# Optimization experiments

Hardware: AMD Instinct MI355X
Metric: run time of the kernel (lower is better)

## Reference

```python
import jax, jax.numpy as jnp
import numpy as np

N, E, C = 50000, 10000, 500
NNZ = 400000
IN_DIM, EDGE_DIM, NODE_DIM, COMP_DIM = 128, 128, 128, 128


def _glorot(key, shape):
    fan = shape[0] + shape[1]
    return jax.random.normal(key, shape, jnp.float32) * (2.0 / fan) ** 0.5


def _seg_mean(vals, idx, num):
    # mean aggregation over segments (scatter-add + count normalize)
    s = jax.ops.segment_sum(vals, idx, num_segments=num)
    cnt = jax.ops.segment_sum(jnp.ones((idx.shape[0], 1), vals.dtype), idx, num_segments=num)
    return s / jnp.maximum(cnt, 1.0)


def _prelu(v, a):
    return jnp.where(v >= 0, v, a * v)


def _conv(x, ni, ei, ec_e, ec_c, nc_n, nc_c, n_nodes, n_edges, n_comps,
          Wne, Wen, Wec, Wnc, a):
    # node -> hyperedge message passing
    e = _seg_mean((x @ Wne)[ni], ei, n_edges)            # [E, edge_dim]
    e_act = _prelu(e, a)
    # hyperedge -> node
    n = _seg_mean((e_act @ Wen)[ei], ni, n_nodes)        # [N, node_dim]
    # edge -> component and node -> component
    c = _seg_mean((e_act @ Wec)[ec_e], ec_c, n_comps) + \
        _seg_mean((x @ Wnc)[nc_n], nc_c, n_comps)        # [C, comp_dim]
    return n, e, c


def setup_inputs() -> dict:
    key = jax.random.key(0)
    ks = jax.random.split(key, 16)
    x = jax.random.normal(ks[0], (N, IN_DIM), jnp.float32)
    hyperedge_index = jnp.stack([
        jax.random.randint(ks[1], (NNZ,), 0, N),
        jax.random.randint(ks[2], (NNZ,), 0, E),
    ])
    hyperedge_component_index = jnp.stack([
        jnp.arange(E), jax.random.randint(ks[3], (E,), 0, C)])
    node_component_index = jnp.stack([
        jnp.arange(N), jax.random.randint(ks[4], (N,), 0, C)])
    return dict(
        x=x,
        hyperedge_index=hyperedge_index,
        hyperedge_component_index=hyperedge_component_index,
        node_component_index=node_component_index,
        num_nodes=N, num_edges=E, num_components=C,
        W_ne0=_glorot(ks[5], (IN_DIM, EDGE_DIM)),
        W_en0=_glorot(ks[6], (EDGE_DIM, NODE_DIM)),
        W_ec0=_glorot(ks[7], (EDGE_DIM, COMP_DIM)),
        W_nc0=_glorot(ks[8], (IN_DIM, COMP_DIM)),
        W_ne1=_glorot(ks[9], (NODE_DIM, EDGE_DIM)),
        W_en1=_glorot(ks[10], (EDGE_DIM, NODE_DIM)),
        W_ec1=_glorot(ks[11], (EDGE_DIM, COMP_DIM)),
        W_nc1=_glorot(ks[12], (NODE_DIM, COMP_DIM)),
        prelu_a=jnp.array(0.25, jnp.float32),
    )


def reference(x, hyperedge_index, hyperedge_component_index, node_component_index,
              num_nodes, num_edges, num_components,
              W_ne0, W_en0, W_ec0, W_nc0, W_ne1, W_en1, W_ec1, W_nc1, prelu_a):
    ni, ei = hyperedge_index[0], hyperedge_index[1]
    ec_e, ec_c = hyperedge_component_index[0], hyperedge_component_index[1]
    nc_n, nc_c = node_component_index[0], node_component_index[1]
    layers = [(W_ne0, W_en0, W_ec0, W_nc0), (W_ne1, W_en1, W_ec1, W_nc1)]
    e_out = c_out = None
    for Wne, Wen, Wec, Wnc in layers:
        n_out, e_out, c_out = _conv(x, ni, ei, ec_e, ec_c, nc_n, nc_c,
                                    num_nodes, num_edges, num_components,
                                    Wne, Wen, Wec, Wnc, prelu_a)
        x = _prelu(n_out, prelu_a)  # HyperEncoder applies act between/after layers
    return (x, e_out, c_out)
```

## Files before the change

### kernel.cpp

```cpp
#include <hip/hip_runtime.h>
#include <stdint.h>

typedef unsigned int u32;
typedef _Float16 f16;
typedef f16 half8 __attribute__((ext_vector_type(8)));
typedef float f32x4 __attribute__((ext_vector_type(4)));
#define TS 4096
#define KB2 256
#define CH 2048

__device__ __forceinline__ float bflo(u32 u) { return __uint_as_float(u << 16); }
__device__ __forceinline__ float bfhi(u32 u) { return __uint_as_float(u & 0xffff0000u); }
__device__ __forceinline__ u32 f2bf(float x) {
    u32 u = __float_as_uint(x);
    return (u + 0x7fffu + ((u >> 16) & 1u)) >> 16;
}
__device__ __forceinline__ u32 pack2(float a, float b) { return f2bf(a) | (f2bf(b) << 16); }

__device__ __forceinline__ int bstart2(int b, int total) {
    return (int)(((unsigned long long)b * (u32)total + KB2 - 1) / KB2);
}

__device__ __forceinline__ int blk_exscan(int v, int& total) {
    __shared__ int ws[5];
    int t = threadIdx.x, lane = t & 63, w = t >> 6;
    int inc = v;
    for (int d = 1; d < 64; d <<= 1) { int u = __shfl_up(inc, d, 64); if (lane >= d) inc += u; }
    __syncthreads();
    if (lane == 63) ws[w] = inc;
    __syncthreads();
    if (t == 0) { int acc = 0; for (int i = 0; i < 4; ++i) { int x = ws[i]; ws[i] = acc; acc += x; } ws[4] = acc; }
    __syncthreads();
    total = ws[4];
    return ws[w] + (inc - v);
}

#define ACC8(v) do { \
    a[0] += bflo((v).x); a[1] += bfhi((v).x); a[2] += bflo((v).y); a[3] += bfhi((v).y); \
    a[4] += bflo((v).z); a[5] += bfhi((v).z); a[6] += bflo((v).w); a[7] += bfhi((v).w); } while (0)

__device__ __forceinline__ void seg_mean8(const u32* __restrict__ in,
                                          const int* __restrict__ items,
                                          const int* __restrict__ off,
                                          int nseg, int nrows, int seg, float a[8]) {
    int lane = threadIdx.x & 63;
    int rs = lane >> 4;
    int cc = lane & 15;
#pragma unroll
    for (int i = 0; i < 8; ++i) a[i] = 0.f;
    int s0 = 0, s1 = 0;
    if (seg < nseg) { s0 = off[seg]; s1 = off[seg + 1]; }
    const uint4* rows = (const uint4*)in;
    int base = s0;
    for (; base + 16 <= s1; base += 16) {
        u32 r0 = (u32)items[base + rs];
        u32 r1 = (u32)items[base + 4 + rs];
        u32 r2 = (u32)items[base + 8 + rs];
        u32 r3 = (u32)items[base + 12 + rs];
        r0 = (r0 < (u32)nrows) ? r0 : 0u;
        r1 = (r1 < (u32)nrows) ? r1 : 0u;
        r2 = (r2 < (u32)nrows) ? r2 : 0u;
        r3 = (r3 < (u32)nrows) ? r3 : 0u;
        uint4 v0 = rows[(size_t)r0 * 16 + cc];
        uint4 v1 = rows[(size_t)r1 * 16 + cc];
        uint4 v2 = rows[(size_t)r2 * 16 + cc];
        uint4 v3 = rows[(size_t)r3 * 16 + cc];
        ACC8(v0); ACC8(v1); ACC8(v2); ACC8(v3);
    }
    for (; base + 8 <= s1; base += 8) {
        u32 r0 = (u32)items[base + rs];
        u32 r1 = (u32)items[base + 4 + rs];
        r0 = (r0 < (u32)nrows) ? r0 : 0u;
        r1 = (r1 < (u32)nrows) ? r1 : 0u;
        uint4 v0 = rows[(size_t)r0 * 16 + cc];
        uint4 v1 = rows[(size_t)r1 * 16 + cc];
        ACC8(v0); ACC8(v1);
    }
    int idx = base + rs;
    if (idx < s1) {
        u32 r = (u32)items[idx]; r = (r < (u32)nrows) ? r : 0u;
        uint4 v = rows[(size_t)r * 16 + cc];
        ACC8(v);
    }
    idx += 4;
    if (idx < s1) {
        u32 r = (u32)items[idx]; r = (r < (u32)nrows) ? r : 0u;
        uint4 v = rows[(size_t)r * 16 + cc];
        ACC8(v);
    }
#pragma unroll
    for (int i = 0; i < 8; ++i) {
        a[i] += __shfl_xor(a[i], 16, 64);
        a[i] += __shfl_xor(a[i], 32, 64);
    }
    float inv = 1.f / fmaxf((float)(s1 - s0), 1.f);
#pragma unroll
    for (int i = 0; i < 8; ++i) a[i] *= inv;
}

__device__ __forceinline__ void agg4_body(const u32* __restrict__ in,
                                          const int* __restrict__ items,
                                          const int* __restrict__ off,
                                          float* __restrict__ out_f32,
                                          u32* __restrict__ out_bf,
                                          int nseg, int nrows, int do_prelu,
                                          const float* __restrict__ alpha_p, int seg) {
    if (seg >= nseg) return;
    int lane = threadIdx.x & 63;
    int rs = lane >> 4;
    int cc = lane & 15;
    float a[8];
    seg_mean8(in, items, off, nseg, nrows, seg, a);
    if (do_prelu) {
        float al = *alpha_p;
#pragma unroll
        for (int i = 0; i < 8; ++i) a[i] = (a[i] >= 0.f) ? a[i] : al * a[i];
    }
    if (rs == 0) {
        if (out_f32) {
            float* o = out_f32 + ((size_t)seg << 7) + cc * 8;
            *(float4*)o       = make_float4(a[0], a[1], a[2], a[3]);
            *(float4*)(o + 4) = make_float4(a[4], a[5], a[6], a[7]);
        }
        if (out_bf) {
            uint4 pk;
            pk.x = pack2(a[0], a[1]); pk.y = pack2(a[2], a[3]);
            pk.z = pack2(a[4], a[5]); pk.w = pack2(a[6], a[7]);
            *(uint4*)(out_bf + ((size_t)seg << 6) + cc * 4) = pk;
        }
    }
}

__global__ __launch_bounds__(256) void k_front(
        const float2* __restrict__ xin, u32* __restrict__ xout, int npairs,
        const int* __restrict__ ni, const int* __restrict__ ei,
        const int* __restrict__ nc_c, const int* __restrict__ ec_c,
        int* __restrict__ bcntE, int* __restrict__ bcntN,
        int* __restrict__ cnt_cn, int* __restrict__ cnt_ce,
        int nnz, int n, int e, int nbh, int nkc,
        int* __restrict__ ticket,
        int* __restrict__ basesE, int* __restrict__ basesN,
        int* __restrict__ bcur_e, int* __restrict__ bcur_n,
        int* __restrict__ off_cn, int* __restrict__ off_ce,
        int* __restrict__ cur_cn, int* __restrict__ cur_ce, int c,
        const float* __restrict__ W0, const float* __restrict__ W1,
        const float* __restrict__ W2, const float* __restrict__ W3,
        const float* __restrict__ W4, const float* __restrict__ W5,
        f16* __restrict__ wt6) {
    int t = threadIdx.x;
    int b = blockIdx.x;
    if (b >= nbh + nkc) {
        int gid = (b - nbh - nkc) * 256 + t;
        if (gid >= 6 * 2048) return;
        int m = gid >> 11;
        int rem = gid & 2047;
        int cq = rem >> 4;
        int s = rem & 15;
        const float* W = (m == 0) ? W0 : (m == 1) ? W1 : (m == 2) ? W2 :
                         (m == 3) ? W3 : (m == 4) ? W4 : W5;
        int khi = ((s & 7) ^ (cq & 7)) | (s & 8);
        int k0 = khi << 3;
        union { f16 h[8]; uint4 v; } u;
#pragma unroll
        for (int j = 0; j < 8; ++j) u.h[j] = (f16)W[((k0 + j) << 7) + cq];
        *(uint4*)(wt6 + ((size_t)m << 14) + (cq << 7) + (s << 3)) = u.v;
        return;
    }
    if (b >= nbh) {
        int j = (b - nbh) * 256 + t;
        if (j < npairs) { float2 v = xin[j]; xout[j] = pack2(v.x, v.y); }
        return;
    }
    __shared__ int hE[KB2], hN[KB2];
    __shared__ int lastflag;
    hE[t] = 0; hN[t] = 0;
    __syncthreads();
    int base = b * CH;
    int lim = base + CH; if (lim > nnz) lim = nnz;
    for (int i = base + t; i < lim; i += 256) {
        u32 v = (u32)ni[i], eg = (u32)ei[i];
        if (v >= (u32)n) v = 0;
        if (eg >= (u32)e) eg = 0;
        atomicAdd(&hE[(int)(((unsigned long long)eg * KB2) / (u32)e)], 1);
        atomicAdd(&hN[(int)(((unsigned long long)v  * KB2) / (u32)n)], 1);
    }
    __syncthreads();
    if (hE[t]) atomicAdd(&bcntE[t], hE[t]);
    if (hN[t]) atomicAdd(&bcntN[t], hN[t]);
    int gid = b * 256 + t, stride = nbh * 256;
    for (int j = gid; j < n + e; j += stride) {
        if (j < n) atomicAdd(&cnt_cn[nc_c[j]], 1);
        else       atomicAdd(&cnt_ce[ec_c[j - n]], 1);
    }
    __syncthreads();
    if (t == 0) {
        __threadfence();
        lastflag = (atomicAdd(ticket, 1) == nbh - 1);
    }
    __syncthreads();
    if (!lastflag) return;
    __threadfence();
    int tot;
    int v = bcntE[t];
    int ex = blk_exscan(v, tot);
    basesE[t] = ex; bcur_e[t] = ex;
    if (t == 0) basesE[KB2] = tot;
    v = bcntN[t];
    ex = blk_exscan(v, tot);
    basesN[t] = ex; bcur_n[t] = ex;
    if (t == 0) basesN[KB2] = tot;
    int i0 = 2 * t, i1 = 2 * t + 1;
    int v0 = (i0 < c) ? cnt_cn[i0] : 0;
    int v1 = (i1 < c) ? cnt_cn[i1] : 0;
    ex = blk_exscan(v0 + v1, tot);
    if (i0 < c) { off_cn[i0] = ex;      cur_cn[i0] = ex; }
    if (i1 < c) { off_cn[i1] = ex + v0; cur_cn[i1] = ex + v0; }
    if (t == 0) off_cn[c] = tot;
    v0 = (i0 < c) ? cnt_ce[i0] : 0;
    v1 = (i1 < c) ? cnt_ce[i1] : 0;
    ex = blk_exscan(v0 + v1, tot);
    if (i0 < c) { off_ce[i0] = ex;      cur_ce[i0] = ex; }
    if (i1 < c) { off_ce[i1] = ex + v0; cur_ce[i1] = ex + v0; }
    if (t == 0) off_ce[c] = tot;
}

__global__ __launch_bounds__(256) void k_part_a(
        const int* __restrict__ ni, const int* __restrict__ ei,
        int* __restrict__ bcur_e, int* __restrict__ bcur_n,
        u32* __restrict__ stg_e, u32* __restrict__ stg_n,
        const int* __restrict__ nc_n, const int* __restrict__ nc_c,
        const int* __restrict__ ec_e, const int* __restrict__ ec_c,
        int* __restrict__ cur_cn, int* __restrict__ cur_ce,
        int* __restrict__ csr_cn, int* __restrict__ csr_ce,
        int nnz, int n, int e) {
    __shared__ u32 pk[CH];
    __shared__ unsigned short bb[CH];
    __shared__ int hist[KB2];
    __shared__ int gb[KB2];
    int side = blockIdx.y;
    int base = blockIdx.x * CH;
    int cnt  = nnz - base; if (cnt > CH) cnt = CH;
    int t = threadIdx.x;
    for (int i = t; i < KB2; i += 256) hist[i] = 0;
    __syncthreads();
    u32 total = side ? (u32)n : (u32)e;
    for (int i = t; i < cnt; i += 256) {
        int v = ni[base + i], eg = ei[base + i];
        u32 key = side ? (u32)v : (u32)eg;
        u32 pay = side ? (u32)eg : (u32)v;
        if (key >= total) key = 0;
        u32 b = (u32)(((unsigned long long)key * KB2) / total);
        pk[i] = side ? (pay | (key << 14)) : (pay | (key << 16));
        bb[i] = (unsigned short)b;
        atomicAdd(&hist[b], 1);
    }
    __syncthreads();
    int* cursor = side ? bcur_n : bcur_e;
    u32* stg    = side ? stg_n  : stg_e;
    if (t < KB2) {
        int h = hist[t];
        gb[t] = h ? atomicAdd(&cursor[t], h) : 0;
        hist[t] = 0;
    }
    __syncthreads();
    for (int i = t; i < cnt; i += 256) {
        int b = bb[i];
        int r = atomicAdd(&hist[b], 1);
        stg[gb[b] + r] = pk[i];
    }
    int gid = blockIdx.x * 256 + t;
    int stride = gridDim.x * 256;
    if (side == 0) {
        for (int j = gid; j < e; j += stride) { int c = ec_c[j]; csr_ce[atomicAdd(&cur_ce[c], 1)] = ec_e[j]; }
    } else {
        for (int j = gid; j < n; j += stride) { int c = nc_c[j]; csr_cn[atomicAdd(&cur_cn[c], 1)] = nc_n[j]; }
    }
}

__global__ __launch_bounds__(256) void k_part_b2(
        const u32* __restrict__ stg_e, const u32* __restrict__ stg_n,
        const int* __restrict__ basesE, const int* __restrict__ basesN,
        int* __restrict__ off_e, int* __restrict__ off_n,
        int* __restrict__ csr_e, int* __restrict__ csr_n, int e, int n) {
    __shared__ int lcnt[256];
    int b = blockIdx.x, t = threadIdx.x;
    const u32* stg; const int* bases; int* off; int* csr; int total; int shift; u32 mask;
    if (b < KB2) { stg = stg_e; bases = basesE; off = off_e; csr = csr_e; total = e; shift = 16; mask = 0xFFFFu; }
    else { b -= KB2; stg = stg_n; bases = basesN; off = off_n; csr = csr_n; total = n; shift = 14; mask = 0x3FFFu; }
    int lo = bstart2(b, total), hi = bstart2(b + 1, total);
    int nid = hi - lo;
    int sbase = bases[b], send = bases[b + 1];
    lcnt[t] = 0;
    __syncthreads();
    for (int i = sbase + t; i < send; i += 256) {
        int key = (int)(stg[i] >> shift);
        atomicAdd(&lcnt[key - lo], 1);
    }
    __syncthreads();
    int cval = (t < nid) ? lcnt[t] : 0;
    int tot;
    int ex = blk_exscan(cval, tot);
    int cursor = sbase + ex;
    if (t < nid) { off[lo + t] = cursor; lcnt[t] = cursor; }
    if (t == 0 && hi == total) off[total] = send;
    __syncthreads();
    for (int i = sbase + t; i < send; i += 256) {
        u32 s = stg[i];
        int key = (int)(s >> shift);
        int pay = (int)(s & mask);
        int p = atomicAdd(&lcnt[key - lo], 1);
        csr[p] = pay;
    }
}

__global__ void k_hist_fb(const int* __restrict__ ni, const int* __restrict__ ei,
                          const int* __restrict__ nc_c, const int* __restrict__ ec_c,
                          int* __restrict__ deg_e, int* __restrict__ deg_n,
                          int* __restrict__ cnt_cn, int* __restrict__ cnt_ce,
                          int nnz, int n, int e) {
    int j = blockIdx.x * blockDim.x + threadIdx.x;
    if (j < nnz) {
        atomicAdd(&deg_e[ei[j]], 1);
        atomicAdd(&deg_n[ni[j]], 1);
    }
    if (j < n) atomicAdd(&cnt_cn[nc_c[j]], 1);
    if (j < e) atomicAdd(&cnt_ce[ec_c[j]], 1);
}

__device__ __forceinline__ void scan_sel(int b, int t0, int t01, int t012,
        const int* c0, int* o0, int* u0, int n0,
        const int* c1, int* o1, int* u1, int n1,
        const int* c2, int* o2, int* u2, int n2,
        const int* c3, int* o3, int* u3, int n3,
        const int*& cnt, int*& off, int*& cur, int& n, int& tile) {
    if (b < t0)        { cnt = c0; off = o0; cur = u0; n = n0; tile = b; }
    else if (b < t01)  { cnt = c1; off = o1; cur = u1; n = n1; tile = b - t0; }
    else if (b < t012) { cnt = c2; off = o2; cur = u2; n = n2; tile = b - t01; }
    else               { cnt = c3; off = o3; cur = u3; n = n3; tile = b - t012; }
}

__global__ void k_scan_p1(const int* c0, int n0, const int* c1, int n1,
                          const int* c2, int n2, const int* c3, int n3,
                          int t0, int t01, int t012, int* __restrict__ tilesum) {
    __shared__ int ws[4];
    int b = blockIdx.x;
    const int* cnt; int* off; int* cur; int n; int tile;
    scan_sel(b, t0, t01, t012, c0, nullptr, nullptr, n0, c1, nullptr, nullptr, n1,
             c2, nullptr, nullptr, n2, c3, nullptr, nullptr, n3, cnt, off, cur, n, tile);
    int base = tile * TS + threadIdx.x * 16;
    int s = 0;
#pragma unroll
    for (int i = 0; i < 16; ++i) { int idx = base + i; if (idx < n) s += cnt[idx]; }
    for (int d = 32; d; d >>= 1) s += __shfl_xor(s, d, 64);
    int lane = threadIdx.x & 63, w = threadIdx.x >> 6;
    if (lane == 0) ws[w] = s;
    __syncthreads();
    if (threadIdx.x == 0) tilesum[b] = ws[0] + ws[1] + ws[2] + ws[3];
}

__global__ void k_scan_p2(const int* __restrict__ tilesum, int* __restrict__ tilebase,
                          int t0, int t01, int t012, int t0123,
                          int* o0, int n0, int* o1, int n1, int* o2, int n2, int* o3, int n3) {
    if (threadIdx.x != 0 || blockIdx.x != 0) return;
    int carry = 0;
    for (int b = 0;    b < t0;    ++b) { tilebase[b] = carry; carry += tilesum[b]; } o0[n0] = carry;
    carry = 0;
    for (int b = t0;   b < t01;   ++b) { tilebase[b] = carry; carry += tilesum[b]; } o1[n1] = carry;
    carry = 0;
    for (int b = t01;  b < t012;  ++b) { tilebase[b] = carry; carry += tilesum[b]; } o2[n2] = carry;
    carry = 0;
    for (int b = t012; b < t0123; ++b) { tilebase[b] = carry; carry += tilesum[b]; } o3[n3] = carry;
}

__global__ void k_scan_p3(const int* c0, int* o0, int* u0, int n0,
                          const int* c1, int* o1, int* u1, int n1,
                          const int* c2, int* o2, int* u2, int n2,
                          const int* c3, int* o3, int* u3, int n3,
                          int t0, int t01, int t012, const int* __restrict__ tilebase) {
    __shared__ int wsum[4];
    int b = blockIdx.x;
    const int* cnt; int* off; int* cur; int n; int tile;
    scan_sel(b, t0, t01, t012, c0, o0, u0, n0, c1, o1, u1, n1,
             c2, o2, u2, n2, c3, o3, u3, n3, cnt, off, cur, n, tile);
    int lane = threadIdx.x & 63, w = threadIdx.x >> 6;
    int base = tile * TS + threadIdx.x * 16;
    int vals[16];
    int s = 0;
#pragma unroll
    for (int i = 0; i < 16; ++i) { int idx = base + i; int v = (idx < n) ? cnt[idx] : 0; vals[i] = v; s += v; }
    int inc = s;
    for (int d = 1; d < 64; d <<= 1) { int u = __shfl_up(inc, d, 64); if (lane >= d) inc += u; }
    if (lane == 63) wsum[w] = inc;
    __syncthreads();
    if (threadIdx.x == 0) {
        int acc = tilebase[b];
        for (int i = 0; i < 4; ++i) { int t = wsum[i]; wsum[i] = acc; acc += t; }
    }
    __syncthreads();
    int ex = wsum[w] + (inc - s);
#pragma unroll
    for (int i = 0; i < 16; ++i) {
        int idx = base + i;
        if (idx < n) { off[idx] = ex; cur[idx] = ex; }
        ex += vals[i];
    }
}

__global__ void k_scatter(const int* __restrict__ ni, const int* __restrict__ ei,
                          const int* __restrict__ nc_n, const int* __restrict__ nc_c,
                          const int* __restrict__ ec_e, const int* __restrict__ ec_c,
                          int* __restrict__ cur_e, int* __restrict__ cur_n,
                          int* __restrict__ cur_cn, int* __restrict__ cur_ce,
                          int* __restrict__ csr_e, int* __restrict__ csr_n,
                          int* __restrict__ csr_cn, int* __restrict__ csr_ce,
                          int nnz, int n, int e) {
    int j = blockIdx.x * blockDim.x + threadIdx.x;
    if (j < nnz) {
        int v = ni[j], eg = ei[j];
        csr_e[atomicAdd(&cur_e[eg], 1)] = v;
        csr_n[atomicAdd(&cur_n[v], 1)] = eg;
    }
    if (j < n) { int c = nc_c[j]; csr_cn[atomicAdd(&cur_cn[c], 1)] = nc_n[j]; }
    if (j < e) { int c = ec_c[j]; csr_ce[atomicAdd(&cur_ce[c], 1)] = ec_e[j]; }
}

__global__ __launch_bounds__(256) void k_agg4(
        const u32* __restrict__ in, const int* __restrict__ items,
        const int* __restrict__ off, float* __restrict__ out_f32,
        u32* __restrict__ out_bf,
        int nseg, int nrows, int do_prelu, const float* __restrict__ alpha_p) {
    int seg = blockIdx.x * (blockDim.x >> 6) + (threadIdx.x >> 6);
    agg4_body(in, items, off, out_f32, out_bf, nseg, nrows, do_prelu, alpha_p, seg);
}

__global__ __launch_bounds__(256) void k_agg_final(
        const u32* __restrict__ ybf, const int* __restrict__ csr_n, const int* __restrict__ off_n,
        float* __restrict__ out_x, int n, int e,
        const u32* __restrict__ eactbf, const int* __restrict__ csr_ce, const int* __restrict__ off_ce,
        float* __restrict__ ca_e,
        const u32* __restrict__ x1bf, const int* __restrict__ csr_cn, const int* __restrict__ off_cn,
        float* __restrict__ ca_n,
        int c, int nblkN, int ncb, const float* __restrict__ alpha_p) {
    int b = blockIdx.x;
    int wv = threadIdx.x >> 6;
    if (b < nblkN) {
        agg4_body(ybf, csr_n, off_n, out_x, nullptr, n, e, 1, alpha_p, b * 4 + wv);
    } else if (b < nblkN + ncb) {
        agg4_body(eactbf, csr_ce, off_ce, ca_e, nullptr, c, e, 0, nullptr, (b - nblkN) * 4 + wv);
    } else {
        agg4_body(x1bf, csr_cn, off_cn, ca_n, nullptr, c, n, 0, nullptr, (b - nblkN - ncb) * 4 + wv);
    }
}

__global__ __launch_bounds__(256) void k_aggmlp(
        const u32* __restrict__ gin, const int* __restrict__ items,
        const int* __restrict__ off, int nseg, int nrows,
        const f16* __restrict__ W1t, const f16* __restrict__ W2t,
        float* __restrict__ out_raw, u32* __restrict__ out_actbf,
        u32* __restrict__ out_ybf, const float* __restrict__ alpha_p) {
    __shared__ f16 As[32 * 128];
    __shared__ f16 Wt[128 * 128];
    int t = threadIdx.x, lane = t & 63, wv = t >> 6;
    int rb = blockIdx.x * 32;
    float al = *alpha_p;
    {
        const uint4* src = (const uint4*)W1t;
        uint4* dst = (uint4*)Wt;
        for (int i = t; i < 2048; i += 256) dst[i] = src[i];
    }
    int rs = lane >> 4, cc = lane & 15;
#pragma unroll 1
    for (int s = 0; s < 8; ++s) {
        int rl = wv * 8 + s;
        float a[8];
        seg_mean8(gin, items, off, nseg, nrows, rb + rl, a);
        if (rs == 0) {
            union { f16 h[8]; uint4 v; } u;
#pragma unroll
            for (int i = 0; i < 8; ++i) u.h[i] = (f16)a[i];
            *(uint4*)((char*)As + (rl << 8) + ((cc << 4) ^ ((rl & 7) << 4))) = u.v;
        }
    }
    __syncthreads();

    int r0q = (wv >> 1) << 4;
    int ctb = (wv & 1) << 2;
    int frow = lane & 15;
    int fk = (lane >> 4) << 3;
    int rl0 = r0q + ((lane >> 4) << 2);
    int ar = r0q + frow;
    int asw = (ar & 7) << 4;

    f32x4 acc[4] = {{0.f,0.f,0.f,0.f},{0.f,0.f,0.f,0.f},{0.f,0.f,0.f,0.f},{0.f,0.f,0.f,0.f}};
#pragma unroll
    for (int ks = 0; ks < 4; ++ks) {
        int kb2 = (ks * 32 + fk) << 1;
        half8 a = *(const half8*)((const char*)As + (ar << 8) + (kb2 ^ asw));
#pragma unroll
        for (int j = 0; j < 4; ++j) {
            int c = ((ctb + j) << 4) + frow;
            half8 b = *(const half8*)((const char*)Wt + (c << 8) + (kb2 ^ ((c & 7) << 4)));
            acc[j] = __builtin_amdgcn_mfma_f32_16x16x32_f16(a, b, acc[j], 0, 0, 0);
        }
    }
    __syncthreads();
    {
        const uint4* src = (const uint4*)W2t;
        uint4* dst = (uint4*)Wt;
        for (int i = t; i < 2048; i += 256) dst[i] = src[i];
    }
#pragma unroll
    for (int j = 0; j < 4; ++j) {
        int c = ((ctb + j) << 4) + frow;
#pragma unroll
        for (int rg = 0; rg < 4; ++rg) {
            int rl = rl0 + rg;
            int row = rb + rl;
            float ev = acc[j][rg];
            if (out_raw != nullptr && row < nseg) out_raw[((size_t)row << 7) + c] = ev;
            float av = (ev >= 0.f) ? ev : al * ev;
            float po = __shfl_xor(av, 1, 64);
            if (out_actbf != nullptr && (frow & 1) == 0 && row < nseg)
                out_actbf[((size_t)row << 6) + (c >> 1)] = pack2(av, po);
            *(f16*)((char*)As + (rl << 8) + (((c << 1)) ^ ((rl & 7) << 4))) = (f16)av;
        }
    }
    __syncthreads();
    f32x4 acc2[4] = {{0.f,0.f,0.f,0.f},{0.f,0.f,0.f,0.f},{0.f,0.f,0.f,0.f},{0.f,0.f,0.f,0.f}};
#pragma unroll
    for (int ks = 0; ks < 4; ++ks) {
        int kb2 = (ks * 32 + fk) << 1;
        half8 a = *(const half8*)((const char*)As + (ar << 8) + (kb2 ^ asw));
#pragma unroll
        for (int j = 0; j < 4; ++j) {
            int c = ((ctb + j) << 4) + frow;
            half8 b = *(const half8*)((const char*)Wt + (c << 8) + (kb2 ^ ((c & 7) << 4)));
            acc2[j] = __builtin_amdgcn_mfma_f32_16x16x32_f16(a, b, acc2[j], 0, 0, 0);
        }
    }
#pragma unroll
    for (int j = 0; j < 4; ++j) {
        int c = ((ctb + j) << 4) + frow;
#pragma unroll
        for (int rg = 0; rg < 4; ++rg) {
            int rl = rl0 + rg;
            int row = rb + rl;
            float yv = acc2[j][rg];
            float po = __shfl_xor(yv, 1, 64);
            if ((frow & 1) == 0 && row < nseg)
                out_ybf[((size_t)row << 6) + (c >> 1)] = pack2(yv, po);
        }
    }
}

__global__ __launch_bounds__(256) void k_gemm_mfma(
        const float* __restrict__ A1, const f16* __restrict__ W1t,
        const float* __restrict__ A2, const f16* __restrict__ W2t,
        float* __restrict__ out, int M) {
    __shared__ f16 Asd[2][32 * 128];
    __shared__ f16 Wt[128 * 128];
    int t = threadIdx.x;
    int rb = blockIdx.x * 32;
    {
        const uint4* src = (const uint4*)W1t;
        uint4* dst = (uint4*)Wt;
        for (int i = t; i < 2048; i += 256) dst[i] = src[i];
    }
    for (int p = 0; p < 2; ++p) {
        const float* Ap = p ? A2 : A1;
        for (int i = t; i < 32 * 32; i += 256) {
            int r = i >> 5, dc = i & 31;
            int row = rb + r;
            float4 v = make_float4(0.f, 0.f, 0.f, 0.f);
            if (row < M) v = *(const float4*)(Ap + ((size_t)row << 7) + dc * 4);
            f16* q = (f16*)((char*)Asd[p] + (r << 8) + ((dc << 3) ^ ((r & 7) << 4)));
            q[0] = (f16)v.x; q[1] = (f16)v.y; q[2] = (f16)v.z; q[3] = (f16)v.w;
        }
    }
    __syncthreads();

    int lane = t & 63, wv = t >> 6;
    int r0  = (wv >> 1) << 4;
    int ctb = (wv & 1) << 2;
    int frow = lane & 15;
    int fk = (lane >> 4) << 3;
    int rl0 = r0 + ((lane >> 4) << 2);
    int ar = r0 + frow;
    int asw = (ar & 7) << 4;

    f32x4 acc[4] = {{0.f,0.f,0.f,0.f},{0.f,0.f,0.f,0.f},{0.f,0.f,0.f,0.f},{0.f,0.f,0.f,0.f}};
#pragma unroll
    for (int ks = 0; ks < 4; ++ks) {
        int kb2 = (ks * 32 + fk) << 1;
        half8 a = *(const half8*)((const char*)Asd[0] + (ar << 8) + (kb2 ^ asw));
#pragma unroll
        for (int j = 0; j < 4; ++j) {
            int c = ((ctb + j) << 4) + frow;
            half8 b = *(const half8*)((const char*)Wt + (c << 8) + (kb2 ^ ((c & 7) << 4)));
            acc[j] = __builtin_amdgcn_mfma_f32_16x16x32_f16(a, b, acc[j], 0, 0, 0);
        }
    }
    __syncthreads();
    {
        const uint4* src = (const uint4*)W2t;
        uint4* dst = (uint4*)Wt;
        for (int i = t; i < 2048; i += 256) dst[i] = src[i];
    }
    __syncthreads();
#pragma unroll
    for (int ks = 0; ks < 4; ++ks) {
        int kb2 = (ks * 32 + fk) << 1;
        half8 a = *(const half8*)((const char*)Asd[1] + (ar << 8) + (kb2 ^ asw));
#pragma unroll
        for (int j = 0; j < 4; ++j) {
            int c = ((ctb + j) << 4) + frow;
            half8 b = *(const half8*)((const char*)Wt + (c << 8) + (kb2 ^ ((c & 7) << 4)));
            acc[j] = __builtin_amdgcn_mfma_f32_16x16x32_f16(a, b, acc[j], 0, 0, 0);
        }
    }
#pragma unroll
    for (int j = 0; j < 4; ++j) {
        int c = ((ctb + j) << 4) + frow;
#pragma unroll
        for (int rg = 0; rg < 4; ++rg) {
            int row = rb + rl0 + rg;
            if (row < M) out[((size_t)row << 7) + c] = acc[j][rg];
        }
    }
}

extern "C" void kernel_launch(void* const* d_in, const int* in_sizes, int n_in,
                              void* d_out, int out_size, void* d_ws, size_t ws_size,
                              hipStream_t stream) {
    const int N   = in_sizes[0] / 128;
    const int NNZ = in_sizes[1] / 2;
    const int E   = in_sizes[2] / 2;
    const int C   = 500;

    const float* x0 = (const float*)d_in[0];
    const int* ni   = (const int*)d_in[1];
    const int* ei   = ni + NNZ;
    const int* ec_e = (const int*)d_in[2];
    const int* ec_c = ec_e + E;
    const int* nc_n = (const int*)d_in[3];
    const int* nc_c = nc_n + N;
    const float* Wne0 = (const float*)d_in[7];
    const float* Wen0 = (const float*)d_in[8];
    const float* Wne1 = (const float*)d_in[11];
    const float* Wen1 = (const float*)d_in[12];
    const float* Wec1 = (const float*)d_in[13];
    const float* Wnc1 = (const float*)d_in[14];
    const float* alpha = (const float*)d_in[15];

    float* out_x = (float*)d_out;
    float* out_e = out_x + (size_t)N * 128;
    float* out_c = out_e + (size_t)E * 128;

    char* w = (char*)d_ws;
    auto alloc = [&](size_t bytes) { char* p = w; w += (bytes + 255) & ~(size_t)255; return p; };
    int* zgrp   = (int*)alloc((size_t)(2 * KB2 + 2 * C + 1) * 4);
    int* bcntE  = zgrp;
    int* bcntN  = zgrp + KB2;
    int* cnt_cn = zgrp + 2 * KB2;
    int* cnt_ce = zgrp + 2 * KB2 + C;
    int* ticket = zgrp + 2 * KB2 + 2 * C;
    int* off_e  = (int*)alloc((size_t)(E + 1) * 4);
    int* off_n  = (int*)alloc((size_t)(N + 1) * 4);
    int* off_cn = (int*)alloc((size_t)(C + 1) * 4);
    int* off_ce = (int*)alloc((size_t)(C + 1) * 4);
    int* cur_cn = (int*)alloc((size_t)C * 4);
    int* cur_ce = (int*)alloc((size_t)C * 4);
    int* csr_e  = (int*)alloc((size_t)NNZ * 4);
    int* csr_n  = (int*)alloc((size_t)NNZ * 4);
    int* csr_cn = (int*)alloc((size_t)N * 4);
    int* csr_ce = (int*)alloc((size_t)E * 4);
    int* basesE = (int*)alloc((size_t)(KB2 + 1) * 4);
    int* basesN = (int*)alloc((size_t)(KB2 + 1) * 4);
    int* bcur_e = (int*)alloc(KB2 * 4);
    int* bcur_n = (int*)alloc(KB2 * 4);
    u32* stg_e  = (u32*)alloc((size_t)NNZ * 4);
    u32* stg_n  = (u32*)alloc((size_t)NNZ * 4);
    u32* xbf    = (u32*)alloc((size_t)N * 64 * 4);
    u32* x1bf   = (u32*)alloc((size_t)N * 64 * 4);
    u32* ybf    = (u32*)alloc((size_t)E * 64 * 4);
    u32* eactbf = (u32*)alloc((size_t)E * 64 * 4);
    float* ca_e = (float*)alloc((size_t)C * 128 * 4);
    float* ca_n = (float*)alloc((size_t)C * 128 * 4);
    f16* wt6    = (f16*)alloc((size_t)6 * 16384 * 2);
    int* deg_e    = (int*)alloc((size_t)E * 4);
    int* deg_n    = (int*)alloc((size_t)N * 4);
    int* cur_e    = (int*)alloc((size_t)E * 4);
    int* cur_n    = (int*)alloc((size_t)N * 4);
    int* tilesum  = (int*)alloc(64 * 4);
    int* tilebase = (int*)alloc(64 * 4);

    const int th = 256;
    const int npairs = N * 64;
    const int nbh = (NNZ + CH - 1) / CH;
    const int nkc = (npairs + th - 1) / th;

    bool binned = (E <= 16384) && (N <= 65536) && (E >= KB2) && (N >= KB2) &&
                  ((N + KB2 - 1) / KB2 <= 256) && (C <= 512);
    const int nbh_eff = binned ? nbh : 0;

    hipMemsetAsync(zgrp, 0, (size_t)(2 * KB2 + 2 * C + 1) * 4, stream);
    k_front<<<nbh_eff + nkc + 48, 256, 0, stream>>>(
        (const float2*)x0, xbf, npairs, ni, ei, nc_c, ec_c,
        bcntE, bcntN, cnt_cn, cnt_ce, NNZ, N, E, nbh_eff, nkc,
        ticket, basesE, basesN, bcur_e, bcur_n,
        off_cn, off_ce, cur_cn, cur_ce, C,
        Wne0, Wen0, Wne1, Wen1, Wec1, Wnc1, wt6);

    if (binned) {
        {
            dim3 ga(nbh, 2);
            k_part_a<<<ga, 256, 0, stream>>>(ni, ei, bcur_e, bcur_n, stg_e, stg_n,
                                             nc_n, nc_c, ec_e, ec_c,
                                             cur_cn, cur_ce, csr_cn, csr_ce, NNZ, N, E);
        }
        k_part_b2<<<2 * KB2, 256, 0, stream>>>(stg_e, stg_n, basesE, basesN,
                                               off_e, off_n, csr_e, csr_n, E, N);
    } else {
        hipMemsetAsync(deg_e, 0, (size_t)E * 4, stream);
        hipMemsetAsync(deg_n, 0, (size_t)N * 4, stream);
        k_hist_fb<<<(NNZ > N + E ? NNZ : N + E) / th + 1, th, 0, stream>>>(
            ni, ei, nc_c, ec_c, deg_e, deg_n, cnt_cn, cnt_ce, NNZ, N, E);
        const int t0 = (E + TS - 1) / TS, t1 = (N + TS - 1) / TS;
        const int t2 = (C + TS - 1) / TS, t3 = (C + TS - 1) / TS;
        const int t01 = t0 + t1, t012 = t01 + t2, t0123 = t012 + t3;
        k_scan_p1<<<t0123, 256, 0, stream>>>(deg_e, E, deg_n, N, cnt_cn, C, cnt_ce, C,
                                             t0, t01, t012, tilesum);
        k_scan_p2<<<1, 64, 0, stream>>>(tilesum, tilebase, t0, t01, t012, t0123,
                                        off_e, E, off_n, N, off_cn, C, off_ce, C);
        k_scan_p3<<<t0123, 256, 0, stream>>>(deg_e, off_e, cur_e, E,
                                             deg_n, off_n, cur_n, N,
                                             cnt_cn, off_cn, cur_cn, C,
                                             cnt_ce, off_ce, cur_ce, C,
                                             t0, t01, t012, tilebase);
        k_scatter<<<(NNZ + th - 1) / th, th, 0, stream>>>(ni, ei, nc_n, nc_c, ec_e, ec_c,
                                                          cur_e, cur_n, cur_cn, cur_ce,
                                                          csr_e, csr_n, csr_cn, csr_ce, NNZ, N, E);
    }

    const int gmlp = (E + 31) / 32;
    k_aggmlp<<<gmlp, 256, 0, stream>>>(xbf, csr_e, off_e, E, N,
                                       wt6, wt6 + 16384, nullptr, nullptr, ybf, alpha);
    k_agg4<<<(N + 3) / 4, 256, 0, stream>>>(ybf, csr_n, off_n, nullptr, x1bf, N, E, 1, alpha);
    k_aggmlp<<<gmlp, 256, 0, stream>>>(x1bf, csr_e, off_e, E, N,
                                       wt6 + 2 * 16384, wt6 + 3 * 16384,
                                       out_e, eactbf, ybf, alpha);
    {
        const int nblkN = (N + 3) / 4;
        const int ncb   = (C + 3) / 4;
        k_agg_final<<<nblkN + 2 * ncb, 256, 0, stream>>>(
            ybf, csr_n, off_n, out_x, N, E,
            eactbf, csr_ce, off_ce, ca_e,
            x1bf,   csr_cn, off_cn, ca_n,
            C, nblkN, ncb, alpha);
    }
    k_gemm_mfma<<<(C + 31) / 32, 256, 0, stream>>>(ca_e, wt6 + 4 * 16384,
                                                   ca_n, wt6 + 5 * 16384, out_c, C);
}
```

Before: 285.0 us.

## Split fused segment-mean+MLP into separate aggregation and MFMA GEMM kernels

The fused kernel that gathered 32 hyperedge means per block and then ran two MFMA GEMMs is split in two. A wide aggregation kernel (4 segments per block) writes fp16 means to a new global buffer, and a separate MFMA kernel loads that tile and runs both GEMMs. This spreads the latency-bound gather across many more blocks instead of 313, at the cost of an extra fp16 round trip through global memory and two more launches. Separately, the x fp32-to-bf16 conversion moves from k_front into the k_part_a grid, with a standalone kernel on the fallback path.

```diff
diff --git a/kernel.cpp b/kernel.cpp
--- a/kernel.cpp
+++ b/kernel.cpp
@@ -132,12 +132,11 @@
 }
 
 __global__ __launch_bounds__(256) void k_front(
-        const float2* __restrict__ xin, u32* __restrict__ xout, int npairs,
         const int* __restrict__ ni, const int* __restrict__ ei,
         const int* __restrict__ nc_c, const int* __restrict__ ec_c,
         int* __restrict__ bcntE, int* __restrict__ bcntN,
         int* __restrict__ cnt_cn, int* __restrict__ cnt_ce,
-        int nnz, int n, int e, int nbh, int nkc,
+        int nnz, int n, int e, int nbh,
         int* __restrict__ ticket,
         int* __restrict__ basesE, int* __restrict__ basesN,
         int* __restrict__ bcur_e, int* __restrict__ bcur_n,
@@ -149,8 +148,8 @@
         f16* __restrict__ wt6) {
     int t = threadIdx.x;
     int b = blockIdx.x;
-    if (b >= nbh + nkc) {
-        int gid = (b - nbh - nkc) * 256 + t;
+    if (b >= nbh) {
+        int gid = (b - nbh) * 256 + t;
         if (gid >= 6 * 2048) return;
         int m = gid >> 11;
         int rem = gid & 2047;
@@ -164,11 +163,6 @@
 #pragma unroll
         for (int j = 0; j < 8; ++j) u.h[j] = (f16)W[((k0 + j) << 7) + cq];
         *(uint4*)(wt6 + ((size_t)m << 14) + (cq << 7) + (s << 3)) = u.v;
-        return;
-    }
-    if (b >= nbh) {
-        int j = (b - nbh) * 256 + t;
-        if (j < npairs) { float2 v = xin[j]; xout[j] = pack2(v.x, v.y); }
         return;
     }
     __shared__ int hE[KB2], hN[KB2];
@@ -232,15 +226,23 @@
         const int* __restrict__ ec_e, const int* __restrict__ ec_c,
         int* __restrict__ cur_cn, int* __restrict__ cur_ce,
         int* __restrict__ csr_cn, int* __restrict__ csr_ce,
-        int nnz, int n, int e) {
+        const float2* __restrict__ xin, u32* __restrict__ xout, int npairs,
+        int nnz, int n, int e, int nbh) {
     __shared__ u32 pk[CH];
     __shared__ unsigned short bb[CH];
     __shared__ int hist[KB2];
     __shared__ int gb[KB2];
-    int side = blockIdx.y;
-    int base = blockIdx.x * CH;
+    int t = threadIdx.x;
+    int bx = blockIdx.x;
+    if (bx >= 2 * nbh) {
+        int j = (bx - 2 * nbh) * 256 + t;
+        if (j < npairs) { float2 v = xin[j]; xout[j] = pack2(v.x, v.y); }
+        return;
+    }
+    int side = bx >= nbh;
+    int pb = side ? bx - nbh : bx;
+    int base = pb * CH;
     int cnt  = nnz - base; if (cnt > CH) cnt = CH;
-    int t = threadIdx.x;
     for (int i = t; i < KB2; i += 256) hist[i] = 0;
     __syncthreads();
     u32 total = side ? (u32)n : (u32)e;
@@ -268,8 +270,8 @@
         int r = atomicAdd(&hist[b], 1);
         stg[gb[b] + r] = pk[i];
     }
-    int gid = blockIdx.x * 256 + t;
-    int stride = gridDim.x * 256;
+    int gid = pb * 256 + t;
+    int stride = nbh * 256;
     if (side == 0) {
         for (int j = gid; j < e; j += stride) { int c = ec_c[j]; csr_ce[atomicAdd(&cur_ce[c], 1)] = ec_e[j]; }
     } else {
@@ -313,6 +315,11 @@
     }
 }
 
+__global__ void k_cvt(const float2* __restrict__ in, u32* __restrict__ out, int npairs) {
+    int j = blockIdx.x * blockDim.x + threadIdx.x;
+    if (j < npairs) { float2 v = in[j]; out[j] = pack2(v.x, v.y); }
+}
+
 __global__ void k_hist_fb(const int* __restrict__ ni, const int* __restrict__ ei,
                           const int* __restrict__ nc_c, const int* __restrict__ ec_c,
                           int* __restrict__ deg_e, int* __restrict__ deg_n,
@@ -431,6 +438,23 @@
         int nseg, int nrows, int do_prelu, const float* __restrict__ alpha_p) {
     int seg = blockIdx.x * (blockDim.x >> 6) + (threadIdx.x >> 6);
     agg4_body(in, items, off, out_f32, out_bf, nseg, nrows, do_prelu, alpha_p, seg);
+}
+
+__global__ __launch_bounds__(256) void k_agg4h(
+        const u32* __restrict__ in, const int* __restrict__ items,
+        const int* __restrict__ off, f16* __restrict__ outh,
+        int nseg, int nrows) {
+    int seg = blockIdx.x * (blockDim.x >> 6) + (threadIdx.x >> 6);
+    if (seg >= nseg) return;
+    float a[8];
+    seg_mean8(in, items, off, nseg, nrows, seg, a);
+    int lane = threadIdx.x & 63, rs = lane >> 4, cc = lane & 15;
+    if (rs == 0) {
+        union { f16 h[8]; uint4 v; } u;
+#pragma unroll
+        for (int i = 0; i < 8; ++i) u.h[i] = (f16)a[i];
+        *(uint4*)(outh + ((size_t)seg << 7) + cc * 8) = u.v;
+    }
 }
 
 __global__ __launch_bounds__(256) void k_agg_final(
@@ -452,15 +476,14 @@
     }
 }
 
-__global__ __launch_bounds__(256) void k_aggmlp(
-        const u32* __restrict__ gin, const int* __restrict__ items,
-        const int* __restrict__ off, int nseg, int nrows,
+__global__ __launch_bounds__(256) void k_mlp_mfma(
+        const f16* __restrict__ Ah,
         const f16* __restrict__ W1t, const f16* __restrict__ W2t,
         float* __restrict__ out_raw, u32* __restrict__ out_actbf,
-        u32* __restrict__ out_ybf, const float* __restrict__ alpha_p) {
+        u32* __restrict__ out_ybf, int M, const float* __restrict__ alpha_p) {
     __shared__ f16 As[32 * 128];
     __shared__ f16 Wt[128 * 128];
-    int t = threadIdx.x, lane = t & 63, wv = t >> 6;
+    int t = threadIdx.x;
     int rb = blockIdx.x * 32;
     float al = *alpha_p;
     {
@@ -468,27 +491,25 @@
         uint4* dst = (uint4*)Wt;
         for (int i = t; i < 2048; i += 256) dst[i] = src[i];
     }
-    int rs = lane >> 4, cc = lane & 15;
-#pragma unroll 1
-    for (int s = 0; s < 8; ++s) {
-        int rl = wv * 8 + s;
-        float a[8];
-        seg_mean8(gin, items, off, nseg, nrows, rb + rl, a);
-        if (rs == 0) {
-            union { f16 h[8]; uint4 v; } u;
-#pragma unroll
-            for (int i = 0; i < 8; ++i) u.h[i] = (f16)a[i];
-            *(uint4*)((char*)As + (rl << 8) + ((cc << 4) ^ ((rl & 7) << 4))) = u.v;
-        }
-    }
-    __syncthreads();
-
-    int r0q = (wv >> 1) << 4;
+    {
+        const uint4* Ag = (const uint4*)Ah;
+        for (int i = t; i < 512; i += 256) {
+            int r = i >> 4, s = i & 15;
+            int row = rb + r;
+            uint4 v = make_uint4(0u, 0u, 0u, 0u);
+            if (row < M) v = Ag[(size_t)row * 16 + s];
+            *(uint4*)((char*)As + (r << 8) + ((s << 4) ^ ((r & 7) << 4))) = v;
+        }
+    }
+    __syncthreads();
+
+    int lane = t & 63, wv = t >> 6;
+    int r0  = (wv >> 1) << 4;
     int ctb = (wv & 1) << 2;
     int frow = lane & 15;
     int fk = (lane >> 4) << 3;
-    int rl0 = r0q + ((lane >> 4) << 2);
-    int ar = r0q + frow;
+    int rl0 = r0 + ((lane >> 4) << 2);
+    int ar = r0 + frow;
     int asw = (ar & 7) << 4;
 
     f32x4 acc[4] = {{0.f,0.f,0.f,0.f},{0.f,0.f,0.f,0.f},{0.f,0.f,0.f,0.f},{0.f,0.f,0.f,0.f}};
@@ -517,10 +538,10 @@
             int rl = rl0 + rg;
             int row = rb + rl;
             float ev = acc[j][rg];
-            if (out_raw != nullptr && row < nseg) out_raw[((size_t)row << 7) + c] = ev;
+            if (out_raw != nullptr && row < M) out_raw[((size_t)row << 7) + c] = ev;
             float av = (ev >= 0.f) ? ev : al * ev;
             float po = __shfl_xor(av, 1, 64);
-            if (out_actbf != nullptr && (frow & 1) == 0 && row < nseg)
+            if (out_actbf != nullptr && (frow & 1) == 0 && row < M)
                 out_actbf[((size_t)row << 6) + (c >> 1)] = pack2(av, po);
             *(f16*)((char*)As + (rl << 8) + (((c << 1)) ^ ((rl & 7) << 4))) = (f16)av;
         }
@@ -547,7 +568,7 @@
             int row = rb + rl;
             float yv = acc2[j][rg];
             float po = __shfl_xor(yv, 1, 64);
-            if ((frow & 1) == 0 && row < nseg)
+            if ((frow & 1) == 0 && row < M)
                 out_ybf[((size_t)row << 6) + (c >> 1)] = pack2(yv, po);
         }
     }
@@ -684,6 +705,7 @@
     u32* x1bf   = (u32*)alloc((size_t)N * 64 * 4);
     u32* ybf    = (u32*)alloc((size_t)E * 64 * 4);
     u32* eactbf = (u32*)alloc((size_t)E * 64 * 4);
+    f16* xah    = (f16*)alloc((size_t)E * 128 * 2);
     float* ca_e = (float*)alloc((size_t)C * 128 * 4);
     float* ca_n = (float*)alloc((size_t)C * 128 * 4);
     f16* wt6    = (f16*)alloc((size_t)6 * 16384 * 2);
@@ -704,25 +726,25 @@
     const int nbh_eff = binned ? nbh : 0;
 
     hipMemsetAsync(zgrp, 0, (size_t)(2 * KB2 + 2 * C + 1) * 4, stream);
-    k_front<<<nbh_eff + nkc + 48, 256, 0, stream>>>(
-        (const float2*)x0, xbf, npairs, ni, ei, nc_c, ec_c,
-        bcntE, bcntN, cnt_cn, cnt_ce, NNZ, N, E, nbh_eff, nkc,
+    k_front<<<nbh_eff + 48, 256, 0, stream>>>(
+        ni, ei, nc_c, ec_c,
+        bcntE, bcntN, cnt_cn, cnt_ce, NNZ, N, E, nbh_eff,
         ticket, basesE, basesN, bcur_e, bcur_n,
         off_cn, off_ce, cur_cn, cur_ce, C,
         Wne0, Wen0, Wne1, Wen1, Wec1, Wnc1, wt6);
 
     if (binned) {
-        {
-            dim3 ga(nbh, 2);
-            k_part_a<<<ga, 256, 0, stream>>>(ni, ei, bcur_e, bcur_n, stg_e, stg_n,
-                                             nc_n, nc_c, ec_e, ec_c,
-                                             cur_cn, cur_ce, csr_cn, csr_ce, NNZ, N, E);
-        }
+        k_part_a<<<2 * nbh + nkc, 256, 0, stream>>>(
+            ni, ei, bcur_e, bcur_n, stg_e, stg_n,
+            nc_n, nc_c, ec_e, ec_c,
+            cur_cn, cur_ce, csr_cn, csr_ce,
+            (const float2*)x0, xbf, npairs, NNZ, N, E, nbh);
         k_part_b2<<<2 * KB2, 256, 0, stream>>>(stg_e, stg_n, basesE, basesN,
                                                off_e, off_n, csr_e, csr_n, E, N);
     } else {
         hipMemsetAsync(deg_e, 0, (size_t)E * 4, stream);
         hipMemsetAsync(deg_n, 0, (size_t)N * 4, stream);
+        k_cvt<<<(npairs + th - 1) / th, th, 0, stream>>>((const float2*)x0, xbf, npairs);
         k_hist_fb<<<(NNZ > N + E ? NNZ : N + E) / th + 1, th, 0, stream>>>(
             ni, ei, nc_c, ec_c, deg_e, deg_n, cnt_cn, cnt_ce, NNZ, N, E);
         const int t0 = (E + TS - 1) / TS, t1 = (N + TS - 1) / TS;
@@ -743,12 +765,12 @@
     }
 
     const int gmlp = (E + 31) / 32;
-    k_aggmlp<<<gmlp, 256, 0, stream>>>(xbf, csr_e, off_e, E, N,
-                                       wt6, wt6 + 16384, nullptr, nullptr, ybf, alpha);
+    k_agg4h<<<(E + 3) / 4, 256, 0, stream>>>(xbf, csr_e, off_e, xah, E, N);
+    k_mlp_mfma<<<gmlp, 256, 0, stream>>>(xah, wt6, wt6 + 16384, nullptr, nullptr, ybf, E, alpha);
     k_agg4<<<(N + 3) / 4, 256, 0, stream>>>(ybf, csr_n, off_n, nullptr, x1bf, N, E, 1, alpha);
-    k_aggmlp<<<gmlp, 256, 0, stream>>>(x1bf, csr_e, off_e, E, N,
-                                       wt6 + 2 * 16384, wt6 + 3 * 16384,
-                                       out_e, eactbf, ybf, alpha);
+    k_agg4h<<<(E + 3) / 4, 256, 0, stream>>>(x1bf, csr_e, off_e, xah, E, N);
+    k_mlp_mfma<<<gmlp, 256, 0, stream>>>(xah, wt6 + 2 * 16384, wt6 + 3 * 16384,
+                                         out_e, eactbf, ybf, E, alpha);
     {
         const int nblkN = (N + 3) / 4;
         const int ncb   = (C + 3) / 4;
```

New measurement: 263.2 us. -7.7%, faster.
